# Optimization experiments

Measured on AMD Instinct MI355X. Metric: run time of the kernel, lower is better.

Reference implementation:

```python
import jax, jax.numpy as jnp
import numpy as np

EPS = 1e-8

def rms_norm(x, scale):
    # norm(2,-1)/sqrt(d); x / (rms + eps) * scale
    d = x.shape[-1]
    norm = jnp.sqrt(jnp.sum(x * x, axis=-1, keepdims=True))
    rms = norm / jnp.sqrt(jnp.asarray(d, x.dtype))
    return scale * (x / (rms + EPS))

def setup_inputs() -> dict:
    key = jax.random.key(0)
    B, N, C, FF = 2, 2048, 1024, 4096
    ks = jax.random.split(key, 12)
    s = 0.02
    return {
        "x":  jax.random.normal(ks[0], (B, N, C), jnp.float32),
        "wq": jax.random.normal(ks[1], (C, C), jnp.float32) * s,
        "bq": jnp.zeros((C,), jnp.float32),
        "wk": jax.random.normal(ks[2], (C, C), jnp.float32) * s,
        "bk": jnp.zeros((C,), jnp.float32),
        "wv": jax.random.normal(ks[3], (C, C), jnp.float32) * s,
        "bv": jnp.zeros((C,), jnp.float32),
        "wo": jax.random.normal(ks[4], (C, C), jnp.float32) * s,
        "bo": jnp.zeros((C,), jnp.float32),
        "scale1": jnp.ones((C,), jnp.float32),
        "scale2": jnp.ones((C,), jnp.float32),
        "w1": jax.random.normal(ks[5], (C, FF), jnp.float32) * s,
        "b1": jnp.zeros((FF,), jnp.float32),
        "w2": jax.random.normal(ks[6], (FF, C), jnp.float32) * s,
        "b2": jnp.zeros((C,), jnp.float32),
    }

def reference(x, wq, bq, wk, bk, wv, bv, wo, bo, scale1, scale2, w1, b1, w2, b2):
    B, N, C = x.shape
    H = 16
    D = C // H

    residual = x
    xn = rms_norm(x, scale1)

    def heads(y):  # [B,N,C] -> [B,H,N,D]
        return y.reshape(B, N, H, D).transpose(0, 2, 1, 3)

    q = heads(xn @ wq + bq)
    k = heads(xn @ wk + bk)
    v = heads(xn @ wv + bv)

    # apply_rotary_pos_emb with cos=sin=1: q' = q - roll(q,1,-1), same for k
    q = q - jnp.roll(q, 1, axis=-1)
    k = k - jnp.roll(k, 1, axis=-1)

    # explicit attention (no causal mask in original)
    scores = jnp.einsum('bhnd,bhmd->bhnm', q, k) / jnp.sqrt(jnp.asarray(D, x.dtype))
    probs = jax.nn.softmax(scores, axis=-1)
    attn = jnp.einsum('bhnm,bhmd->bhnd', probs, v)
    attn = attn.transpose(0, 2, 1, 3).reshape(B, N, C)
    attn = attn @ wo + bo

    x = residual + attn
    residual = x
    xn = rms_norm(x, scale2)
    h = jax.nn.gelu(xn @ w1 + b1, approximate=False)  # torch GELU default = exact
    ffn_out = h @ w2 + b2
    return residual + ffn_out
```

## Files before the change

### kernel.cpp

```cpp
#include <hip/hip_runtime.h>
#include <hip/hip_bf16.h>
#include <math.h>

typedef unsigned short u16;
typedef short s16x8 __attribute__((ext_vector_type(8)));
typedef __bf16 bf16x8v __attribute__((ext_vector_type(8)));
typedef float f32x4 __attribute__((ext_vector_type(4)));
typedef unsigned short u16x4 __attribute__((ext_vector_type(4)));

struct Ptr4 { float* p[4]; };
struct TW4 { const float* w[4]; u16* o[4]; int mode[4]; };

__device__ __forceinline__ u16 f2b(float f) {
    __hip_bfloat16 h = __float2bfloat16(f);
    return __builtin_bit_cast(u16, h);
}

__device__ __forceinline__ f32x4 mfma16(s16x8 a, s16x8 b, f32x4 c) {
    return __builtin_amdgcn_mfma_f32_16x16x32_bf16(
        __builtin_bit_cast(bf16x8v, a), __builtin_bit_cast(bf16x8v, b), c, 0, 0, 0);
}

__device__ __forceinline__ void gl_lds16(const void* g, void* l) {
    typedef const unsigned int __attribute__((address_space(1))) * gp_t;
    typedef unsigned int __attribute__((address_space(3))) * lp_t;
    __builtin_amdgcn_global_load_lds((gp_t)(unsigned long long)g,
                                     (lp_t)(unsigned int)(unsigned long long)l,
                                     16, 0, 0);
}

__device__ __forceinline__ float gelu_fast(float v) {
    float u = 1.5957691216f * (v + 0.044715f * v * v * v);
    return v / (1.f + __expf(-u));
}

__global__ __launch_bounds__(256) void transpose_w(const float* __restrict__ W,
                                                   u16* __restrict__ Wt,
                                                   int K, int N) {
    __shared__ u16 tile[32][33];
    const int tx = threadIdx.x & 31, ty = threadIdx.x >> 5;
    const int n0 = blockIdx.x * 32, k0 = blockIdx.y * 32;
#pragma unroll
    for (int i = 0; i < 32; i += 8)
        tile[ty + i][tx] = f2b(W[(size_t)(k0 + ty + i) * N + n0 + tx]);
    __syncthreads();
#pragma unroll
    for (int i = 0; i < 32; i += 8)
        Wt[(size_t)(n0 + ty + i) * K + k0 + tx] = tile[tx][ty + i];
}

__global__ __launch_bounds__(256) void transpose_w4(TW4 io) {
    __shared__ u16 tile[32][33];
    const int z = blockIdx.z;
    const float* W = io.w[z];
    u16* Wt = io.o[z];
    const int mode = io.mode[z];
    const int tx = threadIdx.x & 31, ty = threadIdx.x >> 5;
    const int n0 = blockIdx.x * 32, k0 = blockIdx.y * 32;
    const int n = n0 + tx;
    const int np = (n & ~63) | ((n + 63) & 63);
    const float s = (mode == 1) ? 0.125f : 1.f;
#pragma unroll
    for (int i = 0; i < 32; i += 8) {
        const size_t r = (size_t)(k0 + ty + i) * 1024;
        float v = W[r + n];
        if (mode) v = (v - W[r + np]) * s;
        tile[ty + i][tx] = f2b(v);
    }
    __syncthreads();
#pragma unroll
    for (int i = 0; i < 32; i += 8)
        Wt[(size_t)(n0 + ty + i) * 1024 + k0 + tx] = tile[tx][ty + i];
}

__global__ __launch_bounds__(256) void prep_bias(const float* __restrict__ bq,
                                                 const float* __restrict__ bk,
                                                 const float* __restrict__ bv,
                                                 float* __restrict__ bqkv) {
    const int i = blockIdx.x * 256 + threadIdx.x;
    const int d = i & 1023;
    const int dp = (d & ~63) | ((d + 63) & 63);
    float v;
    if (i < 1024) v = 0.125f * (bq[d] - bq[dp]);
    else if (i < 2048) v = bk[d] - bk[dp];
    else v = bv[d];
    bqkv[i] = v;
}

__global__ __launch_bounds__(256) void transpose_v(const u16* __restrict__ qkv,
                                                   u16* __restrict__ vT) {
    __shared__ u16 tile[32][33];
    const int tx = threadIdx.x & 31, ty = threadIdx.x >> 5;
    const int n0 = blockIdx.x * 32, d0 = blockIdx.y * 32, bh = blockIdx.z;
    const int b = bh >> 4, h = bh & 15;
#pragma unroll
    for (int i = 0; i < 32; i += 8)
        tile[ty + i][tx] =
            qkv[(size_t)(b * 2048 + n0 + ty + i) * 3072 + 2048 + h * 64 + d0 + tx];
    __syncthreads();
#pragma unroll
    for (int i = 0; i < 32; i += 8)
        vT[((size_t)bh * 64 + d0 + ty + i) * 2048 + n0 + tx] = tile[tx][ty + i];
}

__global__ __launch_bounds__(256) void rmsnorm_kernel(const float* __restrict__ x,
                                                      const float* __restrict__ scale,
                                                      u16* __restrict__ out) {
    __shared__ float red[4];
    const int t = threadIdx.x, row = blockIdx.x;
    const float4* xr = (const float4*)(x + (size_t)row * 1024);
    float4 v = xr[t];
    float ss = v.x * v.x + v.y * v.y + v.z * v.z + v.w * v.w;
#pragma unroll
    for (int off = 1; off < 64; off <<= 1) ss += __shfl_xor(ss, off);
    if ((t & 63) == 0) red[t >> 6] = ss;
    __syncthreads();
    float tot = red[0] + red[1] + red[2] + red[3];
    float inv = 1.f / (sqrtf(tot * (1.f / 1024.f)) + 1e-8f);
    const float4* sr = (const float4*)scale;
    float4 s = sr[t];
    u16x4 o;
    o[0] = f2b(v.x * inv * s.x);
    o[1] = f2b(v.y * inv * s.y);
    o[2] = f2b(v.z * inv * s.z);
    o[3] = f2b(v.w * inv * s.w);
    ((u16x4*)(out + (size_t)row * 1024))[t] = o;
}

template <int EPI>
__global__ __launch_bounds__(256) void gemm_kernel(const u16* __restrict__ A,
                                                   const u16* __restrict__ Bt,
                                                   const float* __restrict__ bias,
                                                   const float* __restrict__ resid,
                                                   void* __restrict__ outp,
                                                   int M, int N, int K) {
    __shared__ __align__(16) u16 As[128 * 32];
    __shared__ __align__(16) u16 Bs[128 * 32];
    const int t = threadIdx.x, lane = t & 63;
    const int w = t >> 6, wm = (w >> 1) * 64, wn = (w & 1) * 64;
    const int c = lane & 15, qd = lane >> 4;
    const int n0 = blockIdx.x * 128, m0 = blockIdx.y * 128;

    const int sch = ((t & 3) ^ ((t >> 3) & 3)) * 8;
    const u16* Ag = A + (size_t)(m0 + (t >> 2)) * K + sch;
    const u16* Bg = Bt + (size_t)(n0 + (t >> 2)) * K + sch;
    const size_t half = (size_t)64 * K;
    const int fsw = ((c >> 1) & 3);

    f32x4 acc[4][4] = {};
    for (int kt = 0; kt < K; kt += 32) {
        __syncthreads();
        gl_lds16(Ag, &As[t * 8]);
        gl_lds16(Ag + half, &As[2048 + t * 8]);
        gl_lds16(Bg, &Bs[t * 8]);
        gl_lds16(Bg + half, &Bs[2048 + t * 8]);
        Ag += 32;
        Bg += 32;
        __syncthreads();
        s16x8 a[4], b[4];
#pragma unroll
        for (int im = 0; im < 4; im++)
            a[im] = *(const s16x8*)&As[(wm + im * 16 + c) * 32 + ((qd ^ fsw) * 8)];
#pragma unroll
        for (int jn = 0; jn < 4; jn++)
            b[jn] = *(const s16x8*)&Bs[(wn + jn * 16 + c) * 32 + ((qd ^ fsw) * 8)];
#pragma unroll
        for (int im = 0; im < 4; im++)
#pragma unroll
            for (int jn = 0; jn < 4; jn++)
                acc[im][jn] = mfma16(a[im], b[jn], acc[im][jn]);
    }

#pragma unroll
    for (int im = 0; im < 4; im++) {
#pragma unroll
        for (int jn = 0; jn < 4; jn++) {
            const int colg = n0 + wn + jn * 16 + c;
            const float bv = bias[colg];
#pragma unroll
            for (int r = 0; r < 4; r++) {
                const int rowg = m0 + wm + im * 16 + qd * 4 + r;
                const size_t off = (size_t)rowg * N + colg;
                float v = acc[im][jn][r] + bv;
                if (EPI == 0) {
                    ((u16*)outp)[off] = f2b(v);
                } else if (EPI == 1) {
                    ((float*)outp)[off] = v + resid[off];
                } else {
                    ((u16*)outp)[off] = f2b(gelu_fast(v));
                }
            }
        }
    }
}

__global__ __launch_bounds__(256) void gemm_splitk(const u16* __restrict__ A,
                                                   const u16* __restrict__ Bt,
                                                   Ptr4 parts,
                                                   int N, int Ktot, int Kc) {
    __shared__ __align__(16) u16 As[128 * 32];
    __shared__ __align__(16) u16 Bs[128 * 32];
    const int t = threadIdx.x, lane = t & 63;
    const int w = t >> 6, wm = (w >> 1) * 64, wn = (w & 1) * 64;
    const int c = lane & 15, qd = lane >> 4;
    const int n0 = blockIdx.x * 128, m0 = blockIdx.y * 128;
    const int z = blockIdx.z;
    float* out = parts.p[z];

    const int sch = ((t & 3) ^ ((t >> 3) & 3)) * 8;
    const u16* Ag = A + (size_t)(m0 + (t >> 2)) * Ktot + z * Kc + sch;
    const u16* Bg = Bt + (size_t)(n0 + (t >> 2)) * Ktot + z * Kc + sch;
    const size_t half = (size_t)64 * Ktot;
    const int fsw = ((c >> 1) & 3);

    f32x4 acc[4][4] = {};
    for (int kt = 0; kt < Kc; kt += 32) {
        __syncthreads();
        gl_lds16(Ag, &As[t * 8]);
        gl_lds16(Ag + half, &As[2048 + t * 8]);
        gl_lds16(Bg, &Bs[t * 8]);
        gl_lds16(Bg + half, &Bs[2048 + t * 8]);
        Ag += 32;
        Bg += 32;
        __syncthreads();
        s16x8 a[4], b[4];
#pragma unroll
        for (int im = 0; im < 4; im++)
            a[im] = *(const s16x8*)&As[(wm + im * 16 + c) * 32 + ((qd ^ fsw) * 8)];
#pragma unroll
        for (int jn = 0; jn < 4; jn++)
            b[jn] = *(const s16x8*)&Bs[(wn + jn * 16 + c) * 32 + ((qd ^ fsw) * 8)];
#pragma unroll
        for (int im = 0; im < 4; im++)
#pragma unroll
            for (int jn = 0; jn < 4; jn++)
                acc[im][jn] = mfma16(a[im], b[jn], acc[im][jn]);
    }

#pragma unroll
    for (int im = 0; im < 4; im++)
#pragma unroll
        for (int jn = 0; jn < 4; jn++) {
            const int colg = n0 + wn + jn * 16 + c;
#pragma unroll
            for (int r = 0; r < 4; r++) {
                const int rowg = m0 + wm + im * 16 + qd * 4 + r;
                out[(size_t)rowg * N + colg] = acc[im][jn][r];
            }
        }
}

template <int S, bool NORM>
__global__ __launch_bounds__(256) void reduce_kernel(Ptr4 parts,
                                                     const float* __restrict__ bias,
                                                     const float* __restrict__ resid,
                                                     const float* __restrict__ scale,
                                                     float* __restrict__ yout,
                                                     u16* __restrict__ xnout) {
    __shared__ float red[4];
    const int t = threadIdx.x, row = blockIdx.x;
    const size_t base = (size_t)row * 1024;
    float4 v = ((const float4*)(resid + base))[t];
    float4 bv = ((const float4*)bias)[t];
    v.x += bv.x; v.y += bv.y; v.z += bv.z; v.w += bv.w;
#pragma unroll
    for (int s = 0; s < S; s++) {
        float4 pv = ((const float4*)(parts.p[s] + base))[t];
        v.x += pv.x; v.y += pv.y; v.z += pv.z; v.w += pv.w;
    }
    ((float4*)(yout + base))[t] = v;
    if (NORM) {
        float ss = v.x * v.x + v.y * v.y + v.z * v.z + v.w * v.w;
#pragma unroll
        for (int off = 1; off < 64; off <<= 1) ss += __shfl_xor(ss, off);
        if ((t & 63) == 0) red[t >> 6] = ss;
        __syncthreads();
        float tot = red[0] + red[1] + red[2] + red[3];
        float inv = 1.f / (sqrtf(tot * (1.f / 1024.f)) + 1e-8f);
        float4 s = ((const float4*)scale)[t];
        u16x4 o;
        o[0] = f2b(v.x * inv * s.x);
        o[1] = f2b(v.y * inv * s.y);
        o[2] = f2b(v.z * inv * s.z);
        o[3] = f2b(v.w * inv * s.w);
        ((u16x4*)(xnout + base))[t] = o;
    }
}

__global__ __launch_bounds__(256, 3) void attn_kernel(const u16* __restrict__ qkv,
                                                      const u16* __restrict__ vT,
                                                      u16* __restrict__ attn) {
    __shared__ __align__(16) u16 Ks[2][64 * 64];
    __shared__ __align__(16) u16 Vs[2][64 * 64];
    __shared__ __align__(16) u16 Ps[4 * 32 * 64];

    const int t = threadIdx.x, lane = t & 63, w = t >> 6;
    const int c = lane & 15, qd = lane >> 4;
    const int bh = blockIdx.y, b = bh >> 4, h = bh & 15;
    const int q0 = blockIdx.x * 128;
    const size_t rowbase = (size_t)b * 2048;

    const u16* kg = qkv + rowbase * 3072 + 1024 + h * 64;
    const u16* vg = vT + (size_t)bh * 64 * 2048;

    const int srow = t >> 3;
    const int sch = (t & 7) ^ (srow & 7);

    const u16* kptr = kg + (size_t)srow * 3072 + sch * 8;
    const u16* vptr = vg + (size_t)srow * 2048 + sch * 8;

    gl_lds16(kptr, &Ks[0][t * 8]);
    gl_lds16(kptr + (size_t)32 * 3072, &Ks[0][2048 + t * 8]);
    gl_lds16(vptr, &Vs[0][t * 8]);
    gl_lds16(vptr + (size_t)32 * 2048, &Vs[0][2048 + t * 8]);

    s16x8 qf[2][2];
    {
        const u16* qg = qkv + (rowbase + q0 + w * 32) * 3072 + h * 64;
#pragma unroll
        for (int im = 0; im < 2; im++)
#pragma unroll
            for (int ks = 0; ks < 2; ks++)
                qf[im][ks] = *(const s16x8*)&qg[(size_t)(im * 16 + c) * 3072 +
                                                ks * 32 + qd * 8];
    }
    __syncthreads();

    float lsum[2][4] = {};
    f32x4 o[2][4] = {};
    u16* Pw = &Ps[w * 32 * 64];

    for (int it = 0; it < 32; it++) {
        const int buf = it & 1;
        const u16* Kb = Ks[buf];
        const u16* Vb = Vs[buf];

        if (it + 1 < 32) {
            u16* Kn = Ks[buf ^ 1];
            u16* Vn = Vs[buf ^ 1];
            const size_t ko = (size_t)(it + 1) * 64 * 3072;
            const size_t vo = (size_t)(it + 1) * 64;
            gl_lds16(kptr + ko, &Kn[t * 8]);
            gl_lds16(kptr + ko + (size_t)32 * 3072, &Kn[2048 + t * 8]);
            gl_lds16(vptr + vo, &Vn[t * 8]);
            gl_lds16(vptr + vo + (size_t)32 * 2048, &Vn[2048 + t * 8]);
        }

        s16x8 kf[2][4], vf[2][4];
#pragma unroll
        for (int ks = 0; ks < 2; ks++)
#pragma unroll
            for (int j = 0; j < 4; j++) {
                const int rrow = j * 16 + c;
                const int sw = ((ks * 4 + qd) ^ (rrow & 7)) * 8;
                kf[ks][j] = *(const s16x8*)&Kb[rrow * 64 + sw];
                vf[ks][j] = *(const s16x8*)&Vb[rrow * 64 + sw];
            }

#pragma unroll
        for (int im = 0; im < 2; im++) {
            f32x4 sc[4] = {};
#pragma unroll
            for (int ks = 0; ks < 2; ks++)
#pragma unroll
                for (int jn = 0; jn < 4; jn++)
                    sc[jn] = mfma16(qf[im][ks], kf[ks][jn], sc[jn]);
#pragma unroll
            for (int r = 0; r < 4; r++) {
                const int prow = im * 16 + qd * 4 + r;
                float s = 0.f;
#pragma unroll
                for (int jn = 0; jn < 4; jn++) {
                    float p = __expf(sc[jn][r]);
                    s += p;
                    Pw[prow * 64 + (((jn * 2 + (c >> 3)) ^ (prow & 7)) * 8) + (c & 7)] =
                        f2b(p);
                }
                lsum[im][r] += s;
            }
        }

#pragma unroll
        for (int im = 0; im < 2; im++)
#pragma unroll
            for (int ks = 0; ks < 2; ks++) {
                s16x8 pf = *(const s16x8*)&Pw[(im * 16 + c) * 64 +
                                              (((ks * 4 + qd) ^ (c & 7)) * 8)];
#pragma unroll
                for (int jd = 0; jd < 4; jd++)
                    o[im][jd] = mfma16(pf, vf[ks][jd], o[im][jd]);
            }
        __syncthreads();
    }

#pragma unroll
    for (int im = 0; im < 2; im++)
#pragma unroll
        for (int r = 0; r < 4; r++)
#pragma unroll
            for (int off2 = 1; off2 < 16; off2 <<= 1)
                lsum[im][r] += __shfl_xor(lsum[im][r], off2);

    const int orow_base = b * 2048 + q0 + w * 32;
#pragma unroll
    for (int im = 0; im < 2; im++)
#pragma unroll
        for (int r = 0; r < 4; r++) {
            const float inv = 1.f / lsum[im][r];
            const int grow = orow_base + im * 16 + qd * 4 + r;
#pragma unroll
            for (int jd = 0; jd < 4; jd++)
                attn[(size_t)grow * 1024 + h * 64 + jd * 16 + c] =
                    f2b(o[im][jd][r] * inv);
        }
}

extern "C" void kernel_launch(void* const* d_in, const int* in_sizes, int n_in,
                              void* d_out, int out_size, void* d_ws, size_t ws_size,
                              hipStream_t stream) {
    const float* x = (const float*)d_in[0];
    const float* wq = (const float*)d_in[1];
    const float* bq = (const float*)d_in[2];
    const float* wk = (const float*)d_in[3];
    const float* bk = (const float*)d_in[4];
    const float* wv = (const float*)d_in[5];
    const float* bv = (const float*)d_in[6];
    const float* wo = (const float*)d_in[7];
    const float* bo = (const float*)d_in[8];
    const float* scale1 = (const float*)d_in[9];
    const float* scale2 = (const float*)d_in[10];
    const float* w1 = (const float*)d_in[11];
    const float* b1 = (const float*)d_in[12];
    const float* w2 = (const float*)d_in[13];
    const float* b2 = (const float*)d_in[14];
    float* out = (float*)d_out;

    char* ws = (char*)d_ws;
    size_t off = 0;
    auto alloc = [&](size_t bytes) -> char* {
        char* p = ws + off;
        off += (bytes + 255) & ~(size_t)255;
        return p;
    };
    u16* wqkvT = (u16*)alloc((size_t)3072 * 1024 * 2);
    u16* woT   = (u16*)alloc((size_t)1024 * 1024 * 2);
    u16* w1T   = (u16*)alloc((size_t)4096 * 1024 * 2);
    u16* w2T   = (u16*)alloc((size_t)1024 * 4096 * 2);
    float* bqkv = (float*)alloc(3072 * 4);
    u16* xn    = (u16*)alloc((size_t)4096 * 1024 * 2);
    u16* qkv   = (u16*)alloc((size_t)4096 * 3072 * 2);
    u16* vT    = (u16*)alloc((size_t)32 * 64 * 2048 * 2);
    u16* attnb = (u16*)alloc((size_t)4096 * 1024 * 2);
    float* y1  = (float*)alloc((size_t)4096 * 1024 * 4);
    u16* hbuf  = (u16*)alloc((size_t)4096 * 4096 * 2);

    const size_t SPLIT = (size_t)4096 * 1024;
    Ptr4 po; po.p[0] = (float*)qkv; po.p[1] = (float*)qkv + SPLIT;
    po.p[2] = nullptr; po.p[3] = nullptr;
    Ptr4 pf; pf.p[0] = (float*)xn; pf.p[1] = (float*)xn + SPLIT;
    pf.p[2] = (float*)xn + 2 * SPLIT; pf.p[3] = (float*)wqkvT;

    dim3 blk(256);

    TW4 tw;
    tw.w[0] = wq; tw.o[0] = wqkvT;                          tw.mode[0] = 1;
    tw.w[1] = wk; tw.o[1] = wqkvT + (size_t)1024 * 1024;    tw.mode[1] = 2;
    tw.w[2] = wv; tw.o[2] = wqkvT + (size_t)2048 * 1024;    tw.mode[2] = 0;
    tw.w[3] = wo; tw.o[3] = woT;                            tw.mode[3] = 0;
    transpose_w4<<<dim3(32, 32, 4), blk, 0, stream>>>(tw);
    transpose_w<<<dim3(128, 32), blk, 0, stream>>>(w1, w1T, 1024, 4096);
    transpose_w<<<dim3(32, 128), blk, 0, stream>>>(w2, w2T, 4096, 1024);
    prep_bias<<<12, blk, 0, stream>>>(bq, bk, bv, bqkv);

    rmsnorm_kernel<<<4096, blk, 0, stream>>>(x, scale1, xn);
    gemm_kernel<0><<<dim3(24, 32), blk, 0, stream>>>(xn, wqkvT, bqkv, nullptr, qkv, 4096, 3072, 1024);
    transpose_v<<<dim3(64, 2, 32), blk, 0, stream>>>(qkv, vT);
    attn_kernel<<<dim3(16, 32), blk, 0, stream>>>(qkv, vT, attnb);
    gemm_splitk<<<dim3(8, 32, 2), blk, 0, stream>>>(attnb, woT, po, 1024, 1024, 512);
    reduce_kernel<2, true><<<4096, blk, 0, stream>>>(po, bo, x, scale2, y1, xn);
    gemm_kernel<2><<<dim3(32, 32), blk, 0, stream>>>(xn, w1T, b1, nullptr, hbuf, 4096, 4096, 1024);
    gemm_splitk<<<dim3(8, 32, 4), blk, 0, stream>>>(hbuf, w2T, pf, 1024, 4096, 1024);
    reduce_kernel<4, false><<<4096, blk, 0, stream>>>(pf, b2, y1, nullptr, out, nullptr);
}
```

Baseline: 403.5 us.

## Double GEMM K-tile to 64 and merge weight/bias prep into one launch

Both GEMM kernels now stage 64-wide K slices per barrier pair instead of 32, using an 8-way XOR swizzle, which halves the number of syncthreads and global-to-LDS rounds per output tile. LDS usage per block doubles to 32 KB, which may lower occupancy. Separately, the four weight-transpose and bias-prep kernels are merged into one launch with a 3D grid, cutting launch overhead but leaving many early-exit blocks idle.

```diff
diff --git a/kernel.cpp b/kernel.cpp
--- a/kernel.cpp
+++ b/kernel.cpp
@@ -9,7 +9,10 @@
 typedef unsigned short u16x4 __attribute__((ext_vector_type(4)));
 
 struct Ptr4 { float* p[4]; };
-struct TW4 { const float* w[4]; u16* o[4]; int mode[4]; };
+struct TW6 {
+    const float* w[6]; u16* o[6]; int mode[6];
+    const float *bq, *bk, *bv; float* bqkv;
+};
 
 __device__ __forceinline__ u16 f2b(float f) {
     __hip_bfloat16 h = __float2bfloat16(f);
@@ -34,35 +37,38 @@
     return v / (1.f + __expf(-u));
 }
 
-__global__ __launch_bounds__(256) void transpose_w(const float* __restrict__ W,
-                                                   u16* __restrict__ Wt,
-                                                   int K, int N) {
+__global__ __launch_bounds__(256) void prep_weights(TW6 io) {
+    const int z = blockIdx.z, bx = blockIdx.x, by = blockIdx.y;
+    const float* W; u16* Wt; int mode = 0, N_, K_, n0, k0;
+    if (z < 4) {
+        if (bx >= 32) {
+            if (z == 0 && bx < 44 && by == 0) {
+                const int i = (bx - 32) * 256 + threadIdx.x;
+                const int d = i & 1023;
+                const int dp = (d & ~63) | ((d + 63) & 63);
+                float v;
+                if (i < 1024) v = 0.125f * (io.bq[d] - io.bq[dp]);
+                else if (i < 2048) v = io.bk[d] - io.bk[dp];
+                else v = io.bv[d];
+                io.bqkv[i] = v;
+            }
+            return;
+        }
+        W = io.w[z]; Wt = io.o[z]; mode = io.mode[z];
+        N_ = 1024; K_ = 1024; n0 = bx * 32; k0 = by * 32;
+    } else if (z == 4) {
+        W = io.w[4]; Wt = io.o[4]; N_ = 4096; K_ = 1024; n0 = bx * 32; k0 = by * 32;
+    } else {
+        W = io.w[5]; Wt = io.o[5]; N_ = 1024; K_ = 4096; n0 = by * 32; k0 = bx * 32;
+    }
     __shared__ u16 tile[32][33];
     const int tx = threadIdx.x & 31, ty = threadIdx.x >> 5;
-    const int n0 = blockIdx.x * 32, k0 = blockIdx.y * 32;
-#pragma unroll
-    for (int i = 0; i < 32; i += 8)
-        tile[ty + i][tx] = f2b(W[(size_t)(k0 + ty + i) * N + n0 + tx]);
-    __syncthreads();
-#pragma unroll
-    for (int i = 0; i < 32; i += 8)
-        Wt[(size_t)(n0 + ty + i) * K + k0 + tx] = tile[tx][ty + i];
-}
-
-__global__ __launch_bounds__(256) void transpose_w4(TW4 io) {
-    __shared__ u16 tile[32][33];
-    const int z = blockIdx.z;
-    const float* W = io.w[z];
-    u16* Wt = io.o[z];
-    const int mode = io.mode[z];
-    const int tx = threadIdx.x & 31, ty = threadIdx.x >> 5;
-    const int n0 = blockIdx.x * 32, k0 = blockIdx.y * 32;
     const int n = n0 + tx;
     const int np = (n & ~63) | ((n + 63) & 63);
     const float s = (mode == 1) ? 0.125f : 1.f;
 #pragma unroll
     for (int i = 0; i < 32; i += 8) {
-        const size_t r = (size_t)(k0 + ty + i) * 1024;
+        const size_t r = (size_t)(k0 + ty + i) * N_;
         float v = W[r + n];
         if (mode) v = (v - W[r + np]) * s;
         tile[ty + i][tx] = f2b(v);
@@ -70,21 +76,7 @@
     __syncthreads();
 #pragma unroll
     for (int i = 0; i < 32; i += 8)
-        Wt[(size_t)(n0 + ty + i) * 1024 + k0 + tx] = tile[tx][ty + i];
-}
-
-__global__ __launch_bounds__(256) void prep_bias(const float* __restrict__ bq,
-                                                 const float* __restrict__ bk,
-                                                 const float* __restrict__ bv,
-                                                 float* __restrict__ bqkv) {
-    const int i = blockIdx.x * 256 + threadIdx.x;
-    const int d = i & 1023;
-    const int dp = (d & ~63) | ((d + 63) & 63);
-    float v;
-    if (i < 1024) v = 0.125f * (bq[d] - bq[dp]);
-    else if (i < 2048) v = bk[d] - bk[dp];
-    else v = bv[d];
-    bqkv[i] = v;
+        Wt[(size_t)(n0 + ty + i) * K_ + k0 + tx] = tile[tx][ty + i];
 }
 
 __global__ __launch_bounds__(256) void transpose_v(const u16* __restrict__ qkv,
@@ -134,41 +126,47 @@
                                                    const float* __restrict__ resid,
                                                    void* __restrict__ outp,
                                                    int M, int N, int K) {
-    __shared__ __align__(16) u16 As[128 * 32];
-    __shared__ __align__(16) u16 Bs[128 * 32];
+    __shared__ __align__(16) u16 As[128 * 64];
+    __shared__ __align__(16) u16 Bs[128 * 64];
     const int t = threadIdx.x, lane = t & 63;
     const int w = t >> 6, wm = (w >> 1) * 64, wn = (w & 1) * 64;
     const int c = lane & 15, qd = lane >> 4;
     const int n0 = blockIdx.x * 128, m0 = blockIdx.y * 128;
 
-    const int sch = ((t & 3) ^ ((t >> 3) & 3)) * 8;
-    const u16* Ag = A + (size_t)(m0 + (t >> 2)) * K + sch;
-    const u16* Bg = Bt + (size_t)(n0 + (t >> 2)) * K + sch;
-    const size_t half = (size_t)64 * K;
-    const int fsw = ((c >> 1) & 3);
+    const int srow = t >> 3;
+    const int sch8 = ((t & 7) ^ (srow & 7)) * 8;
+    const u16* Ag = A + (size_t)(m0 + srow) * K + sch8;
+    const u16* Bg = Bt + (size_t)(n0 + srow) * K + sch8;
+    const size_t rstride = (size_t)32 * K;
 
     f32x4 acc[4][4] = {};
-    for (int kt = 0; kt < K; kt += 32) {
-        __syncthreads();
-        gl_lds16(Ag, &As[t * 8]);
-        gl_lds16(Ag + half, &As[2048 + t * 8]);
-        gl_lds16(Bg, &Bs[t * 8]);
-        gl_lds16(Bg + half, &Bs[2048 + t * 8]);
-        Ag += 32;
-        Bg += 32;
-        __syncthreads();
-        s16x8 a[4], b[4];
-#pragma unroll
-        for (int im = 0; im < 4; im++)
-            a[im] = *(const s16x8*)&As[(wm + im * 16 + c) * 32 + ((qd ^ fsw) * 8)];
-#pragma unroll
-        for (int jn = 0; jn < 4; jn++)
-            b[jn] = *(const s16x8*)&Bs[(wn + jn * 16 + c) * 32 + ((qd ^ fsw) * 8)];
-#pragma unroll
-        for (int im = 0; im < 4; im++)
+    for (int kt = 0; kt < K; kt += 64) {
+        __syncthreads();
+#pragma unroll
+        for (int g = 0; g < 4; g++) {
+            gl_lds16(Ag + g * rstride, &As[t * 8 + g * 2048]);
+            gl_lds16(Bg + g * rstride, &Bs[t * 8 + g * 2048]);
+        }
+        Ag += 64;
+        Bg += 64;
+        __syncthreads();
+#pragma unroll
+        for (int s = 0; s < 2; s++) {
+            s16x8 a[4], b[4];
+#pragma unroll
+            for (int im = 0; im < 4; im++)
+                a[im] = *(const s16x8*)&As[(wm + im * 16 + c) * 64 +
+                                           (((s * 4 + qd) ^ (c & 7)) * 8)];
 #pragma unroll
             for (int jn = 0; jn < 4; jn++)
-                acc[im][jn] = mfma16(a[im], b[jn], acc[im][jn]);
+                b[jn] = *(const s16x8*)&Bs[(wn + jn * 16 + c) * 64 +
+                                           (((s * 4 + qd) ^ (c & 7)) * 8)];
+#pragma unroll
+            for (int im = 0; im < 4; im++)
+#pragma unroll
+                for (int jn = 0; jn < 4; jn++)
+                    acc[im][jn] = mfma16(a[im], b[jn], acc[im][jn]);
+        }
     }
 
 #pragma unroll
@@ -198,8 +196,8 @@
                                                    const u16* __restrict__ Bt,
                                                    Ptr4 parts,
                                                    int N, int Ktot, int Kc) {
-    __shared__ __align__(16) u16 As[128 * 32];
-    __shared__ __align__(16) u16 Bs[128 * 32];
+    __shared__ __align__(16) u16 As[128 * 64];
+    __shared__ __align__(16) u16 Bs[128 * 64];
     const int t = threadIdx.x, lane = t & 63;
     const int w = t >> 6, wm = (w >> 1) * 64, wn = (w & 1) * 64;
     const int c = lane & 15, qd = lane >> 4;
@@ -207,34 +205,40 @@
     const int z = blockIdx.z;
     float* out = parts.p[z];
 
-    const int sch = ((t & 3) ^ ((t >> 3) & 3)) * 8;
-    const u16* Ag = A + (size_t)(m0 + (t >> 2)) * Ktot + z * Kc + sch;
-    const u16* Bg = Bt + (size_t)(n0 + (t >> 2)) * Ktot + z * Kc + sch;
-    const size_t half = (size_t)64 * Ktot;
-    const int fsw = ((c >> 1) & 3);
+    const int srow = t >> 3;
+    const int sch8 = ((t & 7) ^ (srow & 7)) * 8;
+    const u16* Ag = A + (size_t)(m0 + srow) * Ktot + z * Kc + sch8;
+    const u16* Bg = Bt + (size_t)(n0 + srow) * Ktot + z * Kc + sch8;
+    const size_t rstride = (size_t)32 * Ktot;
 
     f32x4 acc[4][4] = {};
-    for (int kt = 0; kt < Kc; kt += 32) {
-        __syncthreads();
-        gl_lds16(Ag, &As[t * 8]);
-        gl_lds16(Ag + half, &As[2048 + t * 8]);
-        gl_lds16(Bg, &Bs[t * 8]);
-        gl_lds16(Bg + half, &Bs[2048 + t * 8]);
-        Ag += 32;
-        Bg += 32;
-        __syncthreads();
-        s16x8 a[4], b[4];
-#pragma unroll
-        for (int im = 0; im < 4; im++)
-            a[im] = *(const s16x8*)&As[(wm + im * 16 + c) * 32 + ((qd ^ fsw) * 8)];
-#pragma unroll
-        for (int jn = 0; jn < 4; jn++)
-            b[jn] = *(const s16x8*)&Bs[(wn + jn * 16 + c) * 32 + ((qd ^ fsw) * 8)];
-#pragma unroll
-        for (int im = 0; im < 4; im++)
+    for (int kt = 0; kt < Kc; kt += 64) {
+        __syncthreads();
+#pragma unroll
+        for (int g = 0; g < 4; g++) {
+            gl_lds16(Ag + g * rstride, &As[t * 8 + g * 2048]);
+            gl_lds16(Bg + g * rstride, &Bs[t * 8 + g * 2048]);
+        }
+        Ag += 64;
+        Bg += 64;
+        __syncthreads();
+#pragma unroll
+        for (int s = 0; s < 2; s++) {
+            s16x8 a[4], b[4];
+#pragma unroll
+            for (int im = 0; im < 4; im++)
+                a[im] = *(const s16x8*)&As[(wm + im * 16 + c) * 64 +
+                                           (((s * 4 + qd) ^ (c & 7)) * 8)];
 #pragma unroll
             for (int jn = 0; jn < 4; jn++)
-                acc[im][jn] = mfma16(a[im], b[jn], acc[im][jn]);
+                b[jn] = *(const s16x8*)&Bs[(wn + jn * 16 + c) * 64 +
+                                           (((s * 4 + qd) ^ (c & 7)) * 8)];
+#pragma unroll
+            for (int im = 0; im < 4; im++)
+#pragma unroll
+                for (int jn = 0; jn < 4; jn++)
+                    acc[im][jn] = mfma16(a[im], b[jn], acc[im][jn]);
+        }
     }
 
 #pragma unroll
@@ -462,15 +466,15 @@
 
     dim3 blk(256);
 
-    TW4 tw;
+    TW6 tw;
     tw.w[0] = wq; tw.o[0] = wqkvT;                          tw.mode[0] = 1;
     tw.w[1] = wk; tw.o[1] = wqkvT + (size_t)1024 * 1024;    tw.mode[1] = 2;
     tw.w[2] = wv; tw.o[2] = wqkvT + (size_t)2048 * 1024;    tw.mode[2] = 0;
     tw.w[3] = wo; tw.o[3] = woT;                            tw.mode[3] = 0;
-    transpose_w4<<<dim3(32, 32, 4), blk, 0, stream>>>(tw);
-    transpose_w<<<dim3(128, 32), blk, 0, stream>>>(w1, w1T, 1024, 4096);
-    transpose_w<<<dim3(32, 128), blk, 0, stream>>>(w2, w2T, 4096, 1024);
-    prep_bias<<<12, blk, 0, stream>>>(bq, bk, bv, bqkv);
+    tw.w[4] = w1; tw.o[4] = w1T;                            tw.mode[4] = 0;
+    tw.w[5] = w2; tw.o[5] = w2T;                            tw.mode[5] = 0;
+    tw.bq = bq; tw.bk = bk; tw.bv = bv; tw.bqkv = bqkv;
+    prep_weights<<<dim3(128, 32, 6), blk, 0, stream>>>(tw);
 
     rmsnorm_kernel<<<4096, blk, 0, stream>>>(x, scale1, xn);
     gemm_kernel<0><<<dim3(24, 32), blk, 0, stream>>>(xn, wqkvT, bqkv, nullptr, qkv, 4096, 3072, 1024);
```

Result: faster. 385.7 us (-4.4%).
